# Kernel optimization log

Hardware: AMD Instinct MI355X
Metric: run time of the kernel (lower is better)

The kernel has to match this reference:

```python
import jax, jax.numpy as jnp
import numpy as np

B, S, D, H = 4, 2048, 512, 8
DH = D // H


def setup_inputs() -> dict:
    key = jax.random.key(0)
    ks = jax.random.split(key, 7)
    scale = 1.0 / np.sqrt(DH)  # mimic nn.Linear init magnitude
    return {
        "x": jax.random.normal(ks[0], (B, S, D), dtype=jnp.float32),
        "Wq": jax.random.normal(ks[1], (H, DH, DH), dtype=jnp.float32) * scale,
        "bq": jax.random.normal(ks[2], (H, DH), dtype=jnp.float32) * scale,
        "Wk": jax.random.normal(ks[3], (H, DH, DH), dtype=jnp.float32) * scale,
        "bk": jax.random.normal(ks[4], (H, DH), dtype=jnp.float32) * scale,
        "Wv": jax.random.normal(ks[5], (H, DH, DH), dtype=jnp.float32) * scale,
        "bv": jax.random.normal(ks[6], (H, DH), dtype=jnp.float32) * scale,
    }


def reference(x, Wq, bq, Wk, bk, Wv, bv):
    # x: [B, S, D] -> per-head slices [B, S, H, DH] (contiguous chunks, as in torch slicing)
    xh = x.reshape(B, S, H, DH)
    # nn.Linear: y = x @ W.T + b, per head. Wq[h] is [out, in].
    q = jnp.einsum("bshd,hed->bshe", xh, Wq) + bq  # [B, S, H, DH]
    k = jnp.einsum("bshd,hed->bshe", xh, Wk) + bk
    v = jnp.einsum("bshd,hed->bshe", xh, Wv) + bv
    scores = jnp.einsum("bshe,bthe->bhst", q, k) / jnp.sqrt(jnp.float32(DH))  # [B, H, S, S]
    attn = jax.nn.softmax(scores, axis=-1)
    out = jnp.einsum("bhst,bthe->bshe", attn, v)  # [B, S, H, DH]
    return out.reshape(B, S, D)  # hstack of head outputs == concat along feature dim
```

## Files before the change

### kernel.cpp

```cpp
#include <hip/hip_runtime.h>
#include <math.h>

#define B_ 4
#define S_ 2048
#define D_ 512
#define H_ 8
#define DH_ 64
#define BH_ (B_*H_)
#define SCALE 0.1803368801111243f

typedef __attribute__((ext_vector_type(4)))  float f32x4;
typedef __attribute__((ext_vector_type(16))) float f32x16;
typedef __attribute__((ext_vector_type(8)))  short bf16x8;
typedef __attribute__((ext_vector_type(4)))  uint  u32x4;

__device__ inline uint rnepk(float a, float b) {
    uint ua = __builtin_bit_cast(uint, a), ub = __builtin_bit_cast(uint, b);
    ua += 0x7FFFu + ((ua >> 16) & 1u);
    ub += 0x7FFFu + ((ub >> 16) & 1u);
    return (ua >> 16) | (ub & 0xFFFF0000u);
}
__device__ inline uint truncpk(float lo, float hi) {
    return __builtin_amdgcn_perm(__builtin_bit_cast(uint, hi),
                                 __builtin_bit_cast(uint, lo), 0x07060302u);
}
__device__ inline f32x16 zero16() {
    f32x16 z;
    #pragma unroll
    for (int i = 0; i < 16; ++i) z[i] = 0.f;
    return z;
}

__global__ __launch_bounds__(256, 2)
void qkv_mfma(const float* __restrict__ x,
              const float* __restrict__ Wq, const float* __restrict__ bq,
              const float* __restrict__ Wk, const float* __restrict__ bk,
              const float* __restrict__ Wv, const float* __restrict__ bv,
              ushort* __restrict__ Qb, ushort* __restrict__ Kb,
              ushort* __restrict__ Vtg)
{
    const int bh = blockIdx.x, b = bh >> 3, h = bh & 7;
    const int s0 = blockIdx.y * 128;
    const int tid = threadIdx.x;
    const int w = tid >> 6, lane = tid & 63, l31 = lane & 31, l5 = lane >> 5;

    __shared__ __align__(16) ushort xs[128 * 64];
    __shared__ __align__(16) ushort wl[3][64 * 64];
    __shared__ __align__(16) ushort bnc[4][2560];

    {
        const int row = tid >> 1, half = tid & 1;
        const float* xr = x + ((size_t)(b * S_ + s0 + row)) * D_ + h * DH_ + half * 32;
        ushort* dst = xs + row * 64;
        #pragma unroll
        for (int i = 0; i < 2; ++i) {
            float4 f0 = *(const float4*)(xr + i * 16);
            float4 f1 = *(const float4*)(xr + i * 16 + 4);
            float4 f2 = *(const float4*)(xr + i * 16 + 8);
            float4 f3 = *(const float4*)(xr + i * 16 + 12);
            uint4 c0, c1;
            c0.x = rnepk(f0.x, f0.y); c0.y = rnepk(f0.z, f0.w);
            c0.z = rnepk(f1.x, f1.y); c0.w = rnepk(f1.z, f1.w);
            c1.x = rnepk(f2.x, f2.y); c1.y = rnepk(f2.z, f2.w);
            c1.z = rnepk(f3.x, f3.y); c1.w = rnepk(f3.z, f3.w);
            const int ch0 = half * 4 + i * 2;
            *(uint4*)(dst + ((ch0 ^ (row & 7)) * 8)) = c0;
            *(uint4*)(dst + (((ch0 + 1) ^ (row & 7)) * 8)) = c1;
        }
    }
    {
        const float* Wm[3] = {Wq, Wk, Wv};
        #pragma unroll
        for (int it = 0; it < 6; ++it) {
            const int mat = it >> 1;
            const int e = (it & 1) * 32 + (tid >> 3), ch = tid & 7;
            const float* p = Wm[mat] + h * DH_ * DH_ + e * DH_ + ch * 8;
            float4 a = *(const float4*)(p);
            float4 c = *(const float4*)(p + 4);
            uint4 u;
            u.x = rnepk(a.x, a.y); u.y = rnepk(a.z, a.w);
            u.z = rnepk(c.x, c.y); u.w = rnepk(c.z, c.w);
            *(uint4*)(&wl[mat][e * 64 + ((ch ^ (e & 7)) * 8)]) = u;
        }
    }
    __syncthreads();

    const int srow = w * 32 + l31;
    bf16x8 xf[4];
    #pragma unroll
    for (int st = 0; st < 4; ++st)
        xf[st] = *(const bf16x8*)(xs + srow * 64 + (((st * 2 + l5) ^ (srow & 7)) * 8));

    ushort* mybnc = &bnc[w][0];

    #pragma unroll
    for (int mat = 0; mat < 2; ++mat) {
        const float* bias = mat ? bk : bq;
        f32x16 acc[2];
        #pragma unroll
        for (int et = 0; et < 2; ++et) {
            acc[et] = zero16();
            const int e = et * 32 + l31;
            #pragma unroll
            for (int st = 0; st < 4; ++st) {
                bf16x8 wf = *(const bf16x8*)(&wl[mat][e * 64 + (((st * 2 + l5) ^ (e & 7)) * 8)]);
                acc[et] = __builtin_amdgcn_mfma_f32_32x32x16_bf16(wf, xf[st], acc[et], 0, 0, 0);
            }
        }
        #pragma unroll
        for (int et = 0; et < 2; ++et)
            #pragma unroll
            for (int rg = 0; rg < 4; ++rg) {
                float4 b4 = *(const float4*)(bias + h * DH_ + et * 32 + rg * 8 + l5 * 4);
                float v0 = acc[et][rg * 4 + 0] + b4.x;
                float v1 = acc[et][rg * 4 + 1] + b4.y;
                float v2 = acc[et][rg * 4 + 2] + b4.z;
                float v3 = acc[et][rg * 4 + 3] + b4.w;
                if (mat == 0) { v0 *= SCALE; v1 *= SCALE; v2 *= SCALE; v3 *= SCALE; }
                uint2 pk;
                pk.x = rnepk(v0, v1); pk.y = rnepk(v2, v3);
                *(uint2*)(mybnc + l31 * 72 + et * 32 + rg * 8 + l5 * 4) = pk;
            }
        ushort* Og = mat ? Kb : Qb;
        #pragma unroll
        for (int i = 0; i < 4; ++i) {
            const int slot = lane + 64 * i;
            const int r = slot >> 3, c = slot & 7;
            uint4 v = *(const uint4*)(mybnc + r * 72 + c * 8);
            *(uint4*)(Og + ((size_t)(bh * S_ + s0 + w * 32 + r)) * DH_ + c * 8) = v;
        }
    }

    {
        f32x16 acc[2];
        #pragma unroll
        for (int et = 0; et < 2; ++et) {
            acc[et] = zero16();
            const int e = et * 32 + l31;
            #pragma unroll
            for (int st = 0; st < 4; ++st) {
                bf16x8 wf = *(const bf16x8*)(&wl[2][e * 64 + (((st * 2 + l5) ^ (e & 7)) * 8)]);
                acc[et] = __builtin_amdgcn_mfma_f32_32x32x16_bf16(xf[st], wf, acc[et], 0, 0, 0);
            }
        }
        const float bvv0 = bv[h * DH_ + l31], bvv1 = bv[h * DH_ + 32 + l31];
        #pragma unroll
        for (int et = 0; et < 2; ++et) {
            const float bb = et ? bvv1 : bvv0;
            #pragma unroll
            for (int rg = 0; rg < 4; ++rg) {
                uint2 pk;
                pk.x = rnepk(acc[et][rg * 4 + 0] + bb, acc[et][rg * 4 + 1] + bb);
                pk.y = rnepk(acc[et][rg * 4 + 2] + bb, acc[et][rg * 4 + 3] + bb);
                *(uint2*)(mybnc + (et * 32 + l31) * 40 + rg * 8 + l5 * 4) = pk;
            }
        }
        #pragma unroll
        for (int i = 0; i < 4; ++i) {
            const int slot = lane + 64 * i;
            const int r = slot >> 2, c = slot & 3;
            uint4 v = *(const uint4*)(mybnc + r * 40 + c * 8);
            *(uint4*)(Vtg + ((size_t)(bh * DH_ + r)) * S_ + s0 + w * 32 + c * 8) = v;
        }
    }
}

__global__ __launch_bounds__(256, 2)
void flash_mfma(const ushort* __restrict__ Qb, const ushort* __restrict__ Kb,
                const ushort* __restrict__ Vtg, float* __restrict__ out)
{
    const int blk = blockIdx.x;
    const int bh = blk & 31, qblk = blk >> 5;
    const int b = bh >> 3, h = bh & 7;
    const int tid = threadIdx.x;
    const int w = tid >> 6, lane = tid & 63, l31 = lane & 31, l5 = lane >> 5;

    __shared__ __align__(16) ushort lds_u[17408];
    ushort* Ks = lds_u;
    ushort* Vs = lds_u + 4096;
    ushort* Pw = lds_u + 8192 + w * (32 * 68);

    const int q0 = qblk * 128 + w * 32;
    bf16x8 qf[4];
    #pragma unroll
    for (int st = 0; st < 4; ++st)
        qf[st] = *(const bf16x8*)(Qb + ((size_t)(bh * S_ + q0 + l31)) * DH_
                                  + st * 16 + l5 * 8);

    f32x16 O[2];
    O[0] = zero16(); O[1] = zero16();
    float lsum = 0.f;

    const ushort* kg = Kb + (size_t)bh * S_ * DH_;
    const ushort* vg = Vtg + (size_t)bh * DH_ * S_;
    const int sr0 = tid >> 3, sc = tid & 7, sr1 = sr0 + 32;

    uint4 kv0 = *(const uint4*)(kg + (size_t)sr0 * DH_ + sc * 8);
    uint4 kv1 = *(const uint4*)(kg + (size_t)sr1 * DH_ + sc * 8);
    uint4 vv0 = *(const uint4*)(vg + (size_t)sr0 * S_ + sc * 8);
    uint4 vv1 = *(const uint4*)(vg + (size_t)sr1 * S_ + sc * 8);
    *(uint4*)(Ks + sr0 * 64 + ((sc ^ (sr0 & 7)) * 8)) = kv0;
    *(uint4*)(Ks + sr1 * 64 + ((sc ^ (sr1 & 7)) * 8)) = kv1;
    *(uint4*)(Vs + sr0 * 64 + ((sc ^ (sr0 & 7)) * 8)) = vv0;
    *(uint4*)(Vs + sr1 * 64 + ((sc ^ (sr1 & 7)) * 8)) = vv1;

    for (int kt = 0; kt < 32; ++kt) {
        __syncthreads();
        if (kt < 31) {
            const size_t ko = (size_t)(kt + 1) * 64 * DH_;
            const int vo = (kt + 1) * 64;
            kv0 = *(const uint4*)(kg + ko + (size_t)sr0 * DH_ + sc * 8);
            kv1 = *(const uint4*)(kg + ko + (size_t)sr1 * DH_ + sc * 8);
            vv0 = *(const uint4*)(vg + (size_t)sr0 * S_ + vo + sc * 8);
            vv1 = *(const uint4*)(vg + (size_t)sr1 * S_ + vo + sc * 8);
        }

        #pragma unroll
        for (int g = 0; g < 2; ++g) {
            const int key = g * 32 + l31;
            bf16x8 kf[4];
            #pragma unroll
            for (int st = 0; st < 4; ++st)
                kf[st] = *(const bf16x8*)(Ks + key * 64 + (((st * 2 + l5) ^ (key & 7)) * 8));
            f32x16 sc_ = zero16();
            #pragma unroll
            for (int st = 0; st < 4; ++st)
                sc_ = __builtin_amdgcn_mfma_f32_32x32x16_bf16(kf[st], qf[st], sc_, 0, 0, 0);
            #pragma unroll
            for (int rg = 0; rg < 4; ++rg) {
                float p0 = __builtin_amdgcn_exp2f(sc_[rg * 4 + 0]);
                float p1 = __builtin_amdgcn_exp2f(sc_[rg * 4 + 1]);
                float p2 = __builtin_amdgcn_exp2f(sc_[rg * 4 + 2]);
                float p3 = __builtin_amdgcn_exp2f(sc_[rg * 4 + 3]);
                lsum += (p0 + p1) + (p2 + p3);
                uint2 pk;
                pk.x = truncpk(p0, p1); pk.y = truncpk(p2, p3);
                *(uint2*)(Pw + l31 * 68 + g * 32 + rg * 8 + l5 * 4) = pk;
            }
        }

        bf16x8 pf[4];
        #pragma unroll
        for (int st = 0; st < 4; ++st) {
            const ushort* pp = Pw + l31 * 68 + st * 16 + l5 * 8;
            uint2 lo = *(const uint2*)(pp);
            uint2 hi = *(const uint2*)(pp + 4);
            u32x4 t; t.x = lo.x; t.y = lo.y; t.z = hi.x; t.w = hi.y;
            pf[st] = __builtin_bit_cast(bf16x8, t);
        }
        #pragma unroll
        for (int dht = 0; dht < 2; ++dht) {
            const int dh = dht * 32 + l31;
            bf16x8 vf[4];
            #pragma unroll
            for (int st = 0; st < 4; ++st)
                vf[st] = *(const bf16x8*)(Vs + dh * 64 + (((st * 2 + l5) ^ (dh & 7)) * 8));
            #pragma unroll
            for (int st = 0; st < 4; ++st)
                O[dht] = __builtin_amdgcn_mfma_f32_32x32x16_bf16(vf[st], pf[st], O[dht], 0, 0, 0);
        }

        __syncthreads();
        if (kt < 31) {
            *(uint4*)(Ks + sr0 * 64 + ((sc ^ (sr0 & 7)) * 8)) = kv0;
            *(uint4*)(Ks + sr1 * 64 + ((sc ^ (sr1 & 7)) * 8)) = kv1;
            *(uint4*)(Vs + sr0 * 64 + ((sc ^ (sr0 & 7)) * 8)) = vv0;
            *(uint4*)(Vs + sr1 * 64 + ((sc ^ (sr1 & 7)) * 8)) = vv1;
        }
    }

    lsum += __shfl_xor(lsum, 32);
    const float linv = 1.0f / lsum;
    #pragma unroll
    for (int dht = 0; dht < 2; ++dht)
        #pragma unroll
        for (int i = 0; i < 16; ++i) O[dht][i] *= linv;

    __syncthreads();
    float* ob = (float*)lds_u + w * (32 * 68);
    #pragma unroll
    for (int dht = 0; dht < 2; ++dht)
        #pragma unroll
        for (int rg = 0; rg < 4; ++rg) {
            f32x4 v4;
            v4[0] = O[dht][rg * 4 + 0];
            v4[1] = O[dht][rg * 4 + 1];
            v4[2] = O[dht][rg * 4 + 2];
            v4[3] = O[dht][rg * 4 + 3];
            *(f32x4*)(ob + l31 * 68 + dht * 32 + rg * 8 + l5 * 4) = v4;
        }
    #pragma unroll
    for (int i = 0; i < 8; ++i) {
        const int slot = lane + 64 * i;
        const int r = slot >> 4, c = slot & 15;
        f32x4 v = *(const f32x4*)(ob + r * 68 + c * 4);
        *(f32x4*)(out + ((size_t)(b * S_ + q0 + r)) * D_ + h * DH_ + c * 4) = v;
    }
}

extern "C" void kernel_launch(void* const* d_in, const int* in_sizes, int n_in,
                              void* d_out, int out_size, void* d_ws, size_t ws_size,
                              hipStream_t stream) {
    const float* x  = (const float*)d_in[0];
    const float* Wq = (const float*)d_in[1];
    const float* bq = (const float*)d_in[2];
    const float* Wk = (const float*)d_in[3];
    const float* bk = (const float*)d_in[4];
    const float* Wv = (const float*)d_in[5];
    const float* bv = (const float*)d_in[6];
    float* outp = (float*)d_out;

    ushort* Qb  = (ushort*)d_ws;
    ushort* Kb  = Qb + (size_t)BH_ * S_ * DH_;
    ushort* Vtg = Kb + (size_t)BH_ * S_ * DH_;

    qkv_mfma<<<dim3(BH_, S_ / 128), 256, 0, stream>>>(x, Wq, bq, Wk, bk, Wv, bv,
                                                      Qb, Kb, Vtg);
    flash_mfma<<<dim3(32 * 16), 256, 0, stream>>>(Qb, Kb, Vtg, outp);
}
```

Measured before the change: 133.3 us.

## Double-buffer K/V tiles, keep P in registers via lane swaps, drop QKV LDS staging

The flash kernel now double-buffers K and V in LDS, which removes one of the two block barriers per key tile. The P matrix is no longer written to LDS and read back as the MFMA operand; it is rearranged in registers with a permlane32 swap, with a shuffle fallback. The QKV projection kernel loads x and the weights straight from global memory into bf16 MFMA fragments instead of staging them through shared memory. These changes aim to cut LDS traffic and synchronisation in the attention inner loop, at the cost of more LDS for the second buffer and redundant weight loads per wave.

```diff
diff --git a/kernel.cpp b/kernel.cpp
--- a/kernel.cpp
+++ b/kernel.cpp
@@ -30,6 +30,29 @@
     for (int i = 0; i < 16; ++i) z[i] = 0.f;
     return z;
 }
+__device__ inline bf16x8 pack8(f32x4 a, f32x4 c) {
+    u32x4 u;
+    u.x = rnepk(a[0], a[1]); u.y = rnepk(a[2], a[3]);
+    u.z = rnepk(c[0], c[1]); u.w = rnepk(c[2], c[3]);
+    return __builtin_bit_cast(bf16x8, u);
+}
+
+#if __has_builtin(__builtin_amdgcn_permlane32_swap)
+__device__ inline void lane32swap(uint& a, uint& b) {
+    typedef __attribute__((ext_vector_type(2))) uint u32x2;
+    u32x2 r = __builtin_amdgcn_permlane32_swap(a, b, false, false);
+    a = r.x; b = r.y;
+}
+#else
+__device__ inline void lane32swap(uint& a, uint& b) {
+    const int l5 = (threadIdx.x & 63) >> 5;
+    uint send = l5 ? a : b;
+    uint recv = __shfl_xor(send, 32);
+    uint an = l5 ? recv : a;
+    uint bn = l5 ? b : recv;
+    a = an; b = bn;
+}
+#endif
 
 __global__ __launch_bounds__(256, 2)
 void qkv_mfma(const float* __restrict__ x,
@@ -44,123 +67,86 @@
     const int tid = threadIdx.x;
     const int w = tid >> 6, lane = tid & 63, l31 = lane & 31, l5 = lane >> 5;
 
-    __shared__ __align__(16) ushort xs[128 * 64];
-    __shared__ __align__(16) ushort wl[3][64 * 64];
     __shared__ __align__(16) ushort bnc[4][2560];
-
-    {
-        const int row = tid >> 1, half = tid & 1;
-        const float* xr = x + ((size_t)(b * S_ + s0 + row)) * D_ + h * DH_ + half * 32;
-        ushort* dst = xs + row * 64;
-        #pragma unroll
-        for (int i = 0; i < 2; ++i) {
-            float4 f0 = *(const float4*)(xr + i * 16);
-            float4 f1 = *(const float4*)(xr + i * 16 + 4);
-            float4 f2 = *(const float4*)(xr + i * 16 + 8);
-            float4 f3 = *(const float4*)(xr + i * 16 + 12);
-            uint4 c0, c1;
-            c0.x = rnepk(f0.x, f0.y); c0.y = rnepk(f0.z, f0.w);
-            c0.z = rnepk(f1.x, f1.y); c0.w = rnepk(f1.z, f1.w);
-            c1.x = rnepk(f2.x, f2.y); c1.y = rnepk(f2.z, f2.w);
-            c1.z = rnepk(f3.x, f3.y); c1.w = rnepk(f3.z, f3.w);
-            const int ch0 = half * 4 + i * 2;
-            *(uint4*)(dst + ((ch0 ^ (row & 7)) * 8)) = c0;
-            *(uint4*)(dst + (((ch0 + 1) ^ (row & 7)) * 8)) = c1;
-        }
-    }
-    {
-        const float* Wm[3] = {Wq, Wk, Wv};
-        #pragma unroll
-        for (int it = 0; it < 6; ++it) {
-            const int mat = it >> 1;
-            const int e = (it & 1) * 32 + (tid >> 3), ch = tid & 7;
-            const float* p = Wm[mat] + h * DH_ * DH_ + e * DH_ + ch * 8;
-            float4 a = *(const float4*)(p);
-            float4 c = *(const float4*)(p + 4);
-            uint4 u;
-            u.x = rnepk(a.x, a.y); u.y = rnepk(a.z, a.w);
-            u.z = rnepk(c.x, c.y); u.w = rnepk(c.z, c.w);
-            *(uint4*)(&wl[mat][e * 64 + ((ch ^ (e & 7)) * 8)]) = u;
-        }
-    }
-    __syncthreads();
+    ushort* mybnc = &bnc[w][0];
 
     const int srow = w * 32 + l31;
+    const float* xr = x + ((size_t)(b * S_ + s0 + srow)) * D_ + h * DH_;
     bf16x8 xf[4];
     #pragma unroll
-    for (int st = 0; st < 4; ++st)
-        xf[st] = *(const bf16x8*)(xs + srow * 64 + (((st * 2 + l5) ^ (srow & 7)) * 8));
-
-    ushort* mybnc = &bnc[w][0];
-
-    #pragma unroll
-    for (int mat = 0; mat < 2; ++mat) {
-        const float* bias = mat ? bk : bq;
-        f32x16 acc[2];
+    for (int st = 0; st < 4; ++st) {
+        f32x4 a = *(const f32x4*)(xr + st * 16 + l5 * 8);
+        f32x4 c = *(const f32x4*)(xr + st * 16 + l5 * 8 + 4);
+        xf[st] = pack8(a, c);
+    }
+
+    const float* Wm[3] = {Wq, Wk, Wv};
+    #pragma unroll
+    for (int mat = 0; mat < 3; ++mat) {
+        bf16x8 wf[2][4];
         #pragma unroll
         for (int et = 0; et < 2; ++et) {
-            acc[et] = zero16();
-            const int e = et * 32 + l31;
+            const float* wr = Wm[mat] + h * DH_ * DH_ + (et * 32 + l31) * DH_;
             #pragma unroll
             for (int st = 0; st < 4; ++st) {
-                bf16x8 wf = *(const bf16x8*)(&wl[mat][e * 64 + (((st * 2 + l5) ^ (e & 7)) * 8)]);
-                acc[et] = __builtin_amdgcn_mfma_f32_32x32x16_bf16(wf, xf[st], acc[et], 0, 0, 0);
-            }
-        }
-        #pragma unroll
-        for (int et = 0; et < 2; ++et)
-            #pragma unroll
-            for (int rg = 0; rg < 4; ++rg) {
-                float4 b4 = *(const float4*)(bias + h * DH_ + et * 32 + rg * 8 + l5 * 4);
-                float v0 = acc[et][rg * 4 + 0] + b4.x;
-                float v1 = acc[et][rg * 4 + 1] + b4.y;
-                float v2 = acc[et][rg * 4 + 2] + b4.z;
-                float v3 = acc[et][rg * 4 + 3] + b4.w;
-                if (mat == 0) { v0 *= SCALE; v1 *= SCALE; v2 *= SCALE; v3 *= SCALE; }
-                uint2 pk;
-                pk.x = rnepk(v0, v1); pk.y = rnepk(v2, v3);
-                *(uint2*)(mybnc + l31 * 72 + et * 32 + rg * 8 + l5 * 4) = pk;
-            }
-        ushort* Og = mat ? Kb : Qb;
-        #pragma unroll
-        for (int i = 0; i < 4; ++i) {
-            const int slot = lane + 64 * i;
-            const int r = slot >> 3, c = slot & 7;
-            uint4 v = *(const uint4*)(mybnc + r * 72 + c * 8);
-            *(uint4*)(Og + ((size_t)(bh * S_ + s0 + w * 32 + r)) * DH_ + c * 8) = v;
-        }
-    }
-
-    {
-        f32x16 acc[2];
-        #pragma unroll
-        for (int et = 0; et < 2; ++et) {
-            acc[et] = zero16();
-            const int e = et * 32 + l31;
-            #pragma unroll
-            for (int st = 0; st < 4; ++st) {
-                bf16x8 wf = *(const bf16x8*)(&wl[2][e * 64 + (((st * 2 + l5) ^ (e & 7)) * 8)]);
-                acc[et] = __builtin_amdgcn_mfma_f32_32x32x16_bf16(xf[st], wf, acc[et], 0, 0, 0);
-            }
-        }
-        const float bvv0 = bv[h * DH_ + l31], bvv1 = bv[h * DH_ + 32 + l31];
-        #pragma unroll
-        for (int et = 0; et < 2; ++et) {
-            const float bb = et ? bvv1 : bvv0;
-            #pragma unroll
-            for (int rg = 0; rg < 4; ++rg) {
-                uint2 pk;
-                pk.x = rnepk(acc[et][rg * 4 + 0] + bb, acc[et][rg * 4 + 1] + bb);
-                pk.y = rnepk(acc[et][rg * 4 + 2] + bb, acc[et][rg * 4 + 3] + bb);
-                *(uint2*)(mybnc + (et * 32 + l31) * 40 + rg * 8 + l5 * 4) = pk;
-            }
-        }
-        #pragma unroll
-        for (int i = 0; i < 4; ++i) {
-            const int slot = lane + 64 * i;
-            const int r = slot >> 2, c = slot & 3;
-            uint4 v = *(const uint4*)(mybnc + r * 40 + c * 8);
-            *(uint4*)(Vtg + ((size_t)(bh * DH_ + r)) * S_ + s0 + w * 32 + c * 8) = v;
+                f32x4 a = *(const f32x4*)(wr + st * 16 + l5 * 8);
+                f32x4 c = *(const f32x4*)(wr + st * 16 + l5 * 8 + 4);
+                wf[et][st] = pack8(a, c);
+            }
+        }
+
+        if (mat < 2) {
+            const float* bias = mat ? bk : bq;
+            #pragma unroll
+            for (int et = 0; et < 2; ++et) {
+                f32x16 acc = zero16();
+                #pragma unroll
+                for (int st = 0; st < 4; ++st)
+                    acc = __builtin_amdgcn_mfma_f32_32x32x16_bf16(wf[et][st], xf[st], acc, 0, 0, 0);
+                #pragma unroll
+                for (int rg = 0; rg < 4; ++rg) {
+                    float4 b4 = *(const float4*)(bias + h * DH_ + et * 32 + rg * 8 + l5 * 4);
+                    float v0 = acc[rg * 4 + 0] + b4.x;
+                    float v1 = acc[rg * 4 + 1] + b4.y;
+                    float v2 = acc[rg * 4 + 2] + b4.z;
+                    float v3 = acc[rg * 4 + 3] + b4.w;
+                    if (mat == 0) { v0 *= SCALE; v1 *= SCALE; v2 *= SCALE; v3 *= SCALE; }
+                    uint2 pk;
+                    pk.x = rnepk(v0, v1); pk.y = rnepk(v2, v3);
+                    *(uint2*)(mybnc + l31 * 72 + et * 32 + rg * 8 + l5 * 4) = pk;
+                }
+            }
+            ushort* Og = mat ? Kb : Qb;
+            #pragma unroll
+            for (int i = 0; i < 4; ++i) {
+                const int slot = lane + 64 * i;
+                const int r = slot >> 3, c = slot & 7;
+                uint4 v = *(const uint4*)(mybnc + r * 72 + c * 8);
+                *(uint4*)(Og + ((size_t)(bh * S_ + s0 + w * 32 + r)) * DH_ + c * 8) = v;
+            }
+        } else {
+            #pragma unroll
+            for (int et = 0; et < 2; ++et) {
+                f32x16 acc = zero16();
+                #pragma unroll
+                for (int st = 0; st < 4; ++st)
+                    acc = __builtin_amdgcn_mfma_f32_32x32x16_bf16(xf[st], wf[et][st], acc, 0, 0, 0);
+                const float bb = bv[h * DH_ + et * 32 + l31];
+                #pragma unroll
+                for (int rg = 0; rg < 4; ++rg) {
+                    uint2 pk;
+                    pk.x = rnepk(acc[rg * 4 + 0] + bb, acc[rg * 4 + 1] + bb);
+                    pk.y = rnepk(acc[rg * 4 + 2] + bb, acc[rg * 4 + 3] + bb);
+                    *(uint2*)(mybnc + (et * 32 + l31) * 40 + rg * 8 + l5 * 4) = pk;
+                }
+            }
+            #pragma unroll
+            for (int i = 0; i < 4; ++i) {
+                const int slot = lane + 64 * i;
+                const int r = slot >> 2, c = slot & 3;
+                uint4 v = *(const uint4*)(mybnc + r * 40 + c * 8);
+                *(uint4*)(Vtg + ((size_t)(bh * DH_ + r)) * S_ + s0 + w * 32 + c * 8) = v;
+            }
         }
     }
 }
@@ -176,9 +162,6 @@
     const int w = tid >> 6, lane = tid & 63, l31 = lane & 31, l5 = lane >> 5;
 
     __shared__ __align__(16) ushort lds_u[17408];
-    ushort* Ks = lds_u;
-    ushort* Vs = lds_u + 4096;
-    ushort* Pw = lds_u + 8192 + w * (32 * 68);
 
     const int q0 = qblk * 128 + w * 32;
     bf16x8 qf[4];
@@ -194,18 +177,23 @@
     const ushort* kg = Kb + (size_t)bh * S_ * DH_;
     const ushort* vg = Vtg + (size_t)bh * DH_ * S_;
     const int sr0 = tid >> 3, sc = tid & 7, sr1 = sr0 + 32;
-
-    uint4 kv0 = *(const uint4*)(kg + (size_t)sr0 * DH_ + sc * 8);
-    uint4 kv1 = *(const uint4*)(kg + (size_t)sr1 * DH_ + sc * 8);
-    uint4 vv0 = *(const uint4*)(vg + (size_t)sr0 * S_ + sc * 8);
-    uint4 vv1 = *(const uint4*)(vg + (size_t)sr1 * S_ + sc * 8);
-    *(uint4*)(Ks + sr0 * 64 + ((sc ^ (sr0 & 7)) * 8)) = kv0;
-    *(uint4*)(Ks + sr1 * 64 + ((sc ^ (sr1 & 7)) * 8)) = kv1;
-    *(uint4*)(Vs + sr0 * 64 + ((sc ^ (sr0 & 7)) * 8)) = vv0;
-    *(uint4*)(Vs + sr1 * 64 + ((sc ^ (sr1 & 7)) * 8)) = vv1;
+    const int swz0 = (sc ^ (sr0 & 7)) * 8, swz1 = (sc ^ (sr1 & 7)) * 8;
+
+    {
+        uint4 k0 = *(const uint4*)(kg + (size_t)sr0 * DH_ + sc * 8);
+        uint4 k1 = *(const uint4*)(kg + (size_t)sr1 * DH_ + sc * 8);
+        uint4 v0 = *(const uint4*)(vg + (size_t)sr0 * S_ + sc * 8);
+        uint4 v1 = *(const uint4*)(vg + (size_t)sr1 * S_ + sc * 8);
+        *(uint4*)(lds_u + sr0 * 64 + swz0) = k0;
+        *(uint4*)(lds_u + sr1 * 64 + swz1) = k1;
+        *(uint4*)(lds_u + 8192 + sr0 * 64 + swz0) = v0;
+        *(uint4*)(lds_u + 8192 + sr1 * 64 + swz1) = v1;
+    }
 
     for (int kt = 0; kt < 32; ++kt) {
         __syncthreads();
+        const int cur = kt & 1, nxt = cur ^ 1;
+        uint4 kv0, kv1, vv0, vv1;
         if (kt < 31) {
             const size_t ko = (size_t)(kt + 1) * 64 * DH_;
             const int vo = (kt + 1) * 64;
@@ -214,18 +202,22 @@
             vv0 = *(const uint4*)(vg + (size_t)sr0 * S_ + vo + sc * 8);
             vv1 = *(const uint4*)(vg + (size_t)sr1 * S_ + vo + sc * 8);
         }
-
+        const ushort* ksb = lds_u + cur * 4096;
+        const ushort* vsb = lds_u + 8192 + cur * 4096;
+
+        bf16x8 pf[4];
         #pragma unroll
         for (int g = 0; g < 2; ++g) {
             const int key = g * 32 + l31;
             bf16x8 kf[4];
             #pragma unroll
             for (int st = 0; st < 4; ++st)
-                kf[st] = *(const bf16x8*)(Ks + key * 64 + (((st * 2 + l5) ^ (key & 7)) * 8));
+                kf[st] = *(const bf16x8*)(ksb + key * 64 + (((st * 2 + l5) ^ (key & 7)) * 8));
             f32x16 sc_ = zero16();
             #pragma unroll
             for (int st = 0; st < 4; ++st)
                 sc_ = __builtin_amdgcn_mfma_f32_32x32x16_bf16(kf[st], qf[st], sc_, 0, 0, 0);
+            uint pr[8];
             #pragma unroll
             for (int rg = 0; rg < 4; ++rg) {
                 float p0 = __builtin_amdgcn_exp2f(sc_[rg * 4 + 0]);
@@ -233,39 +225,38 @@
                 float p2 = __builtin_amdgcn_exp2f(sc_[rg * 4 + 2]);
                 float p3 = __builtin_amdgcn_exp2f(sc_[rg * 4 + 3]);
                 lsum += (p0 + p1) + (p2 + p3);
-                uint2 pk;
-                pk.x = truncpk(p0, p1); pk.y = truncpk(p2, p3);
-                *(uint2*)(Pw + l31 * 68 + g * 32 + rg * 8 + l5 * 4) = pk;
-            }
-        }
-
-        bf16x8 pf[4];
-        #pragma unroll
-        for (int st = 0; st < 4; ++st) {
-            const ushort* pp = Pw + l31 * 68 + st * 16 + l5 * 8;
-            uint2 lo = *(const uint2*)(pp);
-            uint2 hi = *(const uint2*)(pp + 4);
-            u32x4 t; t.x = lo.x; t.y = lo.y; t.z = hi.x; t.w = hi.y;
-            pf[st] = __builtin_bit_cast(bf16x8, t);
-        }
+                pr[2 * rg + 0] = truncpk(p0, p1);
+                pr[2 * rg + 1] = truncpk(p2, p3);
+            }
+            #pragma unroll
+            for (int p = 0; p < 2; ++p) {
+                lane32swap(pr[4 * p + 0], pr[4 * p + 2]);
+                lane32swap(pr[4 * p + 1], pr[4 * p + 3]);
+                u32x4 u; u.x = pr[4 * p + 0]; u.y = pr[4 * p + 1];
+                u.z = pr[4 * p + 2]; u.w = pr[4 * p + 3];
+                pf[g * 2 + p] = __builtin_bit_cast(bf16x8, u);
+            }
+        }
+
         #pragma unroll
         for (int dht = 0; dht < 2; ++dht) {
             const int dh = dht * 32 + l31;
             bf16x8 vf[4];
             #pragma unroll
             for (int st = 0; st < 4; ++st)
-                vf[st] = *(const bf16x8*)(Vs + dh * 64 + (((st * 2 + l5) ^ (dh & 7)) * 8));
+                vf[st] = *(const bf16x8*)(vsb + dh * 64 + (((st * 2 + l5) ^ (dh & 7)) * 8));
             #pragma unroll
             for (int st = 0; st < 4; ++st)
                 O[dht] = __builtin_amdgcn_mfma_f32_32x32x16_bf16(vf[st], pf[st], O[dht], 0, 0, 0);
         }
 
-        __syncthreads();
         if (kt < 31) {
-            *(uint4*)(Ks + sr0 * 64 + ((sc ^ (sr0 & 7)) * 8)) = kv0;
-            *(uint4*)(Ks + sr1 * 64 + ((sc ^ (sr1 & 7)) * 8)) = kv1;
-            *(uint4*)(Vs + sr0 * 64 + ((sc ^ (sr0 & 7)) * 8)) = vv0;
-            *(uint4*)(Vs + sr1 * 64 + ((sc ^ (sr1 & 7)) * 8)) = vv1;
+            ushort* kn = lds_u + nxt * 4096;
+            ushort* vn = lds_u + 8192 + nxt * 4096;
+            *(uint4*)(kn + sr0 * 64 + swz0) = kv0;
+            *(uint4*)(kn + sr1 * 64 + swz1) = kv1;
+            *(uint4*)(vn + sr0 * 64 + swz0) = vv0;
+            *(uint4*)(vn + sr1 * 64 + swz1) = vv1;
         }
     }
 
```

New measurement: 134.8 us. About the same (+1.1%).
